# Kernel optimization log

Hardware: AMD Instinct MI355X
Metric: run time of the kernel (lower is better)

## Reference

```python
import jax, jax.numpy as jnp
import numpy as np

B, S = 256, 500
NQ, DQ, DV, M, F = 10000, 128, 256, 50, 512


def _kaiming(key, shape, fan_in):
    return jax.random.normal(key, shape, dtype=jnp.float32) * np.sqrt(2.0 / fan_in)


def setup_inputs() -> dict:
    key = jax.random.key(0)
    ks = jax.random.split(key, 24)
    inp = {
        'q_data': jax.random.randint(ks[0], (B, S), 0, NQ, dtype=jnp.int32),
        'qa_data': jax.random.randint(ks[1], (B, S), 0, 2 * NQ, dtype=jnp.int32),
        'target': jax.random.randint(ks[2], (B, S), 0, 3, dtype=jnp.int32),
        'time_data': jax.random.randint(ks[3], (B, S), 0, 9902, dtype=jnp.int32),
        'attempt_data': jax.random.randint(ks[4], (B, S), 0, 4000, dtype=jnp.int32),
        'hint_data': jax.random.randint(ks[5], (B, S), 0, 60, dtype=jnp.int32),
        'hintTotal_data': jax.random.randint(ks[6], (B, S), 0, 60, dtype=jnp.int32),
    }
    # embedding tables (padding row 0 zeroed, as in torch padding_idx=0)
    inp['q_emb'] = _kaiming(ks[7], (NQ + 1, DQ), DQ).at[0].set(0.0)
    inp['qa_emb'] = _kaiming(ks[8], (2 * NQ + 1, DV), DV).at[0].set(0.0)
    inp['time_emb'] = _kaiming(ks[9], (9902, DQ), DQ).at[0].set(0.0)
    inp['attempt_emb'] = _kaiming(ks[10], (4000, DQ), DQ).at[0].set(0.0)
    inp['hint_total_emb'] = _kaiming(ks[11], (60, DQ), DQ).at[0].set(0.0)
    # memory init
    inp['Mk'] = _kaiming(ks[12], (M, DQ), DQ)
    inp['Mv0'] = _kaiming(ks[13], (M, DV), DV)
    # difficulty linears (shared weights applied twice)
    inp['diff_W'] = _kaiming(ks[14], (DQ, DQ), DQ)
    inp['diff_b'] = jnp.zeros((DQ,), jnp.float32)
    inp['diff2_W'] = _kaiming(ks[15], (DQ, DQ), DQ)
    inp['diff2_b'] = jnp.zeros((DQ,), jnp.float32)
    # DKVMN write head: erase/add linears (DV -> DV)
    inp['erase_W'] = _kaiming(ks[16], (DV, DV), DV)
    inp['erase_b'] = jnp.zeros((DV,), jnp.float32)
    inp['add_W'] = _kaiming(ks[17], (DV, DV), DV)
    inp['add_b'] = jnp.zeros((DV,), jnp.float32)
    # readout
    inp['read_W'] = _kaiming(ks[18], (F, DV + DQ), DV + DQ)
    inp['read_b'] = jnp.zeros((F,), jnp.float32)
    inp['pred_W'] = _kaiming(ks[19], (1, F), F)
    inp['pred_b'] = jnp.zeros((1,), jnp.float32)
    return inp


def reference(q_data, qa_data, target, time_data, attempt_data, hint_data, hintTotal_data,
              q_emb, qa_emb, time_emb, attempt_emb, hint_total_emb,
              Mk, Mv0, diff_W, diff_b, diff2_W, diff2_b,
              erase_W, erase_b, add_W, add_b, read_W, read_b, pred_W, pred_b):
    lin1 = lambda x: x @ diff_W.T + diff_b
    lin2 = lambda x: x @ diff2_W.T + diff2_b

    qe = q_emb[q_data]                        # [B,S,DQ]
    te = time_emb[time_data]
    ae = attempt_emb[attempt_data]
    he = hint_total_emb[hint_data]            # forward uses hint_total_embed for both
    hte = hint_total_emb[hintTotal_data]

    time_final = jax.nn.sigmoid(lin2(jnp.tanh(lin1(te + qe))))
    diff_final = jax.nn.sigmoid(lin2(jnp.tanh(lin1(hte + he + ae + qe))))
    q_proc = lin1(qe + diff_final * (he + hte + ae))  # [B,S,DQ]
    qa_e = qa_emb[qa_data]                            # [B,S,DV]

    Mv_init = jnp.broadcast_to(Mv0[None], (q_data.shape[0], M, DV))

    def step(Mv, inp):
        q, qa = inp                                   # [B,DQ], [B,DV]
        w = jax.nn.softmax(q @ Mk.T, axis=-1)         # [B,M]
        read = jnp.einsum('bm,bmd->bd', w, Mv)        # [B,DV]
        e = jax.nn.sigmoid(qa @ erase_W.T + erase_b)  # [B,DV]
        a = jnp.tanh(qa @ add_W.T + add_b)            # [B,DV]
        Mv = Mv * (1.0 - w[:, :, None] * e[:, None, :]) + w[:, :, None] * a[:, None, :]
        return Mv, read

    _, reads = jax.lax.scan(step, Mv_init,
                            (jnp.swapaxes(q_proc, 0, 1), jnp.swapaxes(qa_e, 0, 1)))
    reads = jnp.swapaxes(reads, 0, 1)                 # [B,S,DV]

    input_embed = q_proc + time_final * te            # [B,S,DQ]
    predict_input = jnp.concatenate([reads, input_embed], axis=-1)
    rc = jnp.tanh(predict_input @ read_W.T + read_b)  # [B,S,F]
    pred = (rc @ pred_W.T + pred_b).reshape(-1)       # [B*S]

    t1 = target.reshape(-1)
    mask = t1 >= 1
    y = jnp.where(mask, t1 - 1, 0).astype(jnp.float32)
    # BCE with logits: log(1+e^x) - x*y
    lelem = jnp.logaddexp(0.0, pred) - pred * y
    n = jnp.maximum(jnp.sum(mask.astype(jnp.float32)), 1.0)
    loss = jnp.sum(jnp.where(mask, lelem, 0.0)) / n
    maskf = mask.astype(jnp.float32)
    return loss, jax.nn.sigmoid(pred) * maskf, y * maskf
```

## Files before the change

### kernel.cpp

```cpp
#include <hip/hip_runtime.h>
#include <cstdint>
#include <cstddef>

#define NB 256
#define SQ 500
#define NROWS (NB * SQ)
#define DQ 128
#define DV 256
#define MM 50
#define FF 512
#define NQA 20096
#define WSTRIDE 52
#define WT 10

typedef _Float16 half8 __attribute__((ext_vector_type(8)));
typedef float floatx4 __attribute__((ext_vector_type(4)));
typedef float f2 __attribute__((ext_vector_type(2)));
typedef unsigned int u32;
typedef unsigned short u16;

typedef __attribute__((address_space(1))) void gvoid;
typedef __attribute__((address_space(3))) void lvoid;

__device__ __forceinline__ void gl16(const u16* g, u16* l) {
    __builtin_amdgcn_global_load_lds((gvoid*)g, (lvoid*)l, 16, 0, 0);
}

__device__ __forceinline__ float4 ld4(const float* p) {
    return *reinterpret_cast<const float4*>(p);
}
__device__ __forceinline__ float sigf(float x) { return 1.f / (1.f + __expf(-x)); }
__device__ __forceinline__ float tanhfast(float x) { return 2.f / (1.f + __expf(-2.f * x)) - 1.f; }
__device__ __forceinline__ int gmap(int l, int s0, int CS) {
    int b = (unsigned)l / (unsigned)CS;
    return b * SQ + s0 + (l - b * CS);
}
__device__ __forceinline__ void st4h(u16* dst, float4 v) {
    _Float16 h0 = (_Float16)v.x, h1 = (_Float16)v.y, h2 = (_Float16)v.z, h3 = (_Float16)v.w;
    ushort4 u;
    u.x = *(u16*)&h0; u.y = *(u16*)&h1; u.z = *(u16*)&h2; u.w = *(u16*)&h3;
    *(ushort4*)dst = u;
}
__device__ __forceinline__ float h2f(u16 b) { _Float16 h; *(u16*)&h = b; return (float)h; }
__device__ __forceinline__ u16 f2h(float x) { _Float16 h = (_Float16)x; return *(u16*)&h; }

__global__ __launch_bounds__(256) void cvt16(
    const float* __restrict__ s, u16* __restrict__ d, int n4)
{
    int i = blockIdx.x * 256 + threadIdx.x;
    if (i < n4) st4h(d + 4 * (size_t)i, ld4(s + 4 * (size_t)i));
}

__global__ __launch_bounds__(256) void mkcvt(
    const float* __restrict__ Mk, u16* __restrict__ Mkh)
{
    int i = blockIdx.x * 256 + threadIdx.x;
    if (i >= 64 * 32) return;
    int row = i >> 5;
    float4 v = (row < MM) ? ld4(Mk + (size_t)row * DQ + (i & 31) * 4)
                          : float4{0.f, 0.f, 0.f, 0.f};
    st4h(Mkh + 4 * (size_t)i, v);
}

__global__ __launch_bounds__(256) void prep128(
    const int* __restrict__ q_data, const int* __restrict__ time_data,
    const int* __restrict__ attempt_data, const int* __restrict__ hint_data,
    const int* __restrict__ hintT_data,
    const float* __restrict__ q_emb, const float* __restrict__ time_emb,
    const float* __restrict__ attempt_emb, const float* __restrict__ ht_emb,
    u16* __restrict__ Xp, u16* __restrict__ S3p, u16* __restrict__ QEp,
    int s0, int CS, int Nc)
{
    int g = blockIdx.x * 256 + threadIdx.x;
    int l = g >> 5;
    int kq = (g & 31) << 2;
    if (l >= Nc) return;
    int n = gmap(l, s0, CS);
    float4 qe  = ld4(q_emb       + (size_t)q_data[n]       * DQ + kq);
    float4 te  = ld4(time_emb    + (size_t)time_data[n]    * DQ + kq);
    float4 ae  = ld4(attempt_emb + (size_t)attempt_data[n] * DQ + kq);
    float4 he  = ld4(ht_emb      + (size_t)hint_data[n]    * DQ + kq);
    float4 hte = ld4(ht_emb      + (size_t)hintT_data[n]   * DQ + kq);
    size_t off = (size_t)l * DQ + kq;
    float4 x1, s3, x2;
    x1.x = te.x + qe.x; x1.y = te.y + qe.y; x1.z = te.z + qe.z; x1.w = te.w + qe.w;
    s3.x = he.x + hte.x + ae.x; s3.y = he.y + hte.y + ae.y;
    s3.z = he.z + hte.z + ae.z; s3.w = he.w + hte.w + ae.w;
    x2.x = s3.x + qe.x; x2.y = s3.y + qe.y; x2.z = s3.z + qe.z; x2.w = s3.w + qe.w;
    st4h(Xp + off, x1);
    st4h(Xp + (size_t)Nc * DQ + off, x2);
    st4h(S3p + off, s3);
    st4h(QEp + off, qe);
}

template <int MODE>
__global__ __launch_bounds__(256, 2) void gemm16(
    const u16* __restrict__ A, const u16* __restrict__ W0,
    const u16* __restrict__ W1, const float* __restrict__ b0,
    const float* __restrict__ b1, u16* __restrict__ Yh,
    float* __restrict__ Yf,
    const u16* __restrict__ QEp, const u16* __restrict__ S3p,
    const int* __restrict__ idx, const float* __restrict__ gtab,
    u16* __restrict__ AUX, const float* __restrict__ predW,
    int K, int Nc, int s0, int CS)
{
    __shared__ u16 smem[2 * 128 * 64];
    u16* At = smem;
    u16* Bt = smem + 128 * 64;
    const int tid = threadIdx.x;
    const int row0 = blockIdx.x * 128;
    const int by = blockIdx.y;

    const u16* Wp;
    int col0;
    if constexpr (MODE == 4) { Wp = (by < 2) ? W0 : W1; col0 = (by & 1) * 128; }
    else { Wp = W0; col0 = by * 128; }
    const float* bias = (MODE == 4 && by >= 2) ? b1 : b0;

    floatx4 acc[4][4];
#pragma unroll
    for (int m = 0; m < 4; ++m)
#pragma unroll
        for (int n = 0; n < 4; ++n) acc[m][n] = (floatx4)0.f;

    const int lane = tid & 63, wv = tid >> 6;
    const int wr = (wv >> 1) * 64, wc = (wv & 1) * 64;
    const int q = lane >> 4, c0 = lane & 15;

    for (int kt = 0; kt < K; kt += 64) {
#pragma unroll
        for (int j = 0; j < 4; ++j) {
            int f = tid + j * 256;
            int r = f >> 3;
            int lg = (f & 7) ^ (r & 7);
            gl16(A + (size_t)(row0 + r) * K + kt + lg * 8, &At[f * 8]);
        }
#pragma unroll
        for (int j = 0; j < 4; ++j) {
            int f = tid + j * 256;
            int r = f >> 3;
            int lg = (f & 7) ^ (r & 7);
            gl16(Wp + (size_t)(col0 + r) * K + kt + lg * 8, &Bt[f * 8]);
        }
        __syncthreads();
#pragma unroll
        for (int kk = 0; kk < 2; ++kk) {
            half8 af[4], bf[4];
#pragma unroll
            for (int m = 0; m < 4; ++m) {
                int row = wr + m * 16 + c0;
                af[m] = *(half8*)&At[row * 64 + ((((kk << 2) | q)) ^ (row & 7)) * 8];
            }
#pragma unroll
            for (int n = 0; n < 4; ++n) {
                int row = wc + n * 16 + c0;
                bf[n] = *(half8*)&Bt[row * 64 + ((((kk << 2) | q)) ^ (row & 7)) * 8];
            }
#pragma unroll
            for (int m = 0; m < 4; ++m)
#pragma unroll
                for (int n = 0; n < 4; ++n)
                    acc[m][n] = __builtin_amdgcn_mfma_f32_16x16x32_f16(af[m], bf[n], acc[m][n], 0, 0, 0);
        }
        __syncthreads();
    }

    float bv[4];
#pragma unroll
    for (int n = 0; n < 4; ++n) bv[n] = bias[col0 + wc + n * 16 + c0];

    if constexpr (MODE == 5) {
        float pw[4];
#pragma unroll
        for (int n = 0; n < 4; ++n) pw[n] = predW[col0 + wc + n * 16 + c0];
        float* red = (float*)smem;
#pragma unroll
        for (int m = 0; m < 4; ++m)
#pragma unroll
            for (int r4 = 0; r4 < 4; ++r4) {
                int row = wr + m * 16 + q * 4 + r4;
                float pp = 0.f;
#pragma unroll
                for (int n = 0; n < 4; ++n)
                    pp = fmaf(tanhfast(acc[m][n][r4] + bv[n]), pw[n], pp);
                red[row * 33 + (wv & 1) * 16 + c0] = pp;
            }
        __syncthreads();
        if (tid < 128) {
            float s = 0.f;
#pragma unroll
            for (int j = 0; j < 32; ++j) s += red[tid * 33 + j];
            atomicAdd(&Yf[row0 + tid], s);
        }
    } else {
#pragma unroll
        for (int m = 0; m < 4; ++m)
#pragma unroll
            for (int r4 = 0; r4 < 4; ++r4) {
                int row = row0 + wr + m * 16 + q * 4 + r4;
#pragma unroll
                for (int n = 0; n < 4; ++n) {
                    int col = col0 + wc + n * 16 + c0;
                    float v = acc[m][n][r4] + bv[n];
                    if constexpr (MODE == 1) {
                        Yh[(size_t)row * 128 + col] = f2h(tanhfast(v));
                    } else if constexpr (MODE == 2) {
                        v = sigf(v);
                        if (row < Nc) {
                            Yh[(size_t)row * 128 + col] = f2h(v);
                        } else {
                            size_t o = (size_t)(row - Nc) * 128 + col;
                            float qe = h2f(QEp[o]), s3 = h2f(S3p[o]);
                            Yh[(size_t)row * 128 + col] = f2h(fmaf(v, s3, qe));
                        }
                    } else if constexpr (MODE == 3) {
                        size_t o = (size_t)row * 128 + col;
                        float tf = h2f(Yh[o]);
                        float te = gtab[(size_t)idx[gmap(row, s0, CS)] * 128 + col];
                        AUX[(size_t)row * 384 + 256 + col] = f2h(fmaf(tf, te, v));
                        Yh[o] = f2h(v);
                    } else {
                        bool isE = (by < 2);
                        v = isE ? sigf(v) : tanhfast(v);
                        AUX[((size_t)row * 256 + col) * 2 + (isE ? 0 : 1)] = f2h(v);
                    }
                }
            }
    }
}

__global__ __launch_bounds__(256) void wsoftmax_mfma(
    const u16* __restrict__ QP, const u16* __restrict__ Mkh,
    float* __restrict__ Wb)
{
    __shared__ float Sred[128 * 67];
    u16* At = (u16*)Sred;
    u16* Bt = At + 128 * 40;
    const int tid = threadIdx.x;
    const int row0 = blockIdx.x * 128;
    const int lane = tid & 63, wv = tid >> 6;
    const int wr = wv * 32;
    const int q = lane >> 4, c0 = lane & 15;

    floatx4 acc[2][4];
#pragma unroll
    for (int m = 0; m < 2; ++m)
#pragma unroll
        for (int n = 0; n < 4; ++n) acc[m][n] = (floatx4)0.f;

    for (int kt = 0; kt < DQ; kt += 32) {
#pragma unroll
        for (int i = 0; i < 3; ++i) {
            int c = tid + i * 256;
            if (c < 512) {
                int r = c >> 2, seg = c & 3;
                *(uint4*)&At[r * 40 + seg * 8] =
                    *(const uint4*)(QP + (size_t)(row0 + r) * DQ + kt + seg * 8);
            } else {
                int cb = c - 512;
                int r = cb >> 2, seg = cb & 3;
                *(uint4*)&Bt[r * 40 + seg * 8] =
                    *(const uint4*)(Mkh + (size_t)r * DQ + kt + seg * 8);
            }
        }
        __syncthreads();
        half8 af[2], bf[4];
#pragma unroll
        for (int m = 0; m < 2; ++m) af[m] = *(half8*)&At[(wr + m * 16 + c0) * 40 + q * 8];
#pragma unroll
        for (int n = 0; n < 4; ++n) bf[n] = *(half8*)&Bt[(n * 16 + c0) * 40 + q * 8];
#pragma unroll
        for (int m = 0; m < 2; ++m)
#pragma unroll
            for (int n = 0; n < 4; ++n)
                acc[m][n] = __builtin_amdgcn_mfma_f32_16x16x32_f16(af[m], bf[n], acc[m][n], 0, 0, 0);
        __syncthreads();
    }

#pragma unroll
    for (int m = 0; m < 2; ++m)
#pragma unroll
        for (int r4 = 0; r4 < 4; ++r4) {
            int row = wr + m * 16 + q * 4 + r4;
#pragma unroll
            for (int n = 0; n < 4; ++n)
                Sred[row * 67 + n * 16 + c0] = acc[m][n][r4];
        }
    __syncthreads();

    if (tid < 128) {
        float* s = &Sred[tid * 67];
        float mx = -3.0e38f;
#pragma unroll
        for (int m = 0; m < MM; ++m) mx = fmaxf(mx, s[m]);
        float sum = 0.f;
#pragma unroll
        for (int m = 0; m < MM; ++m) { float e = __expf(s[m] - mx); s[m] = e; sum += e; }
        float inv = 1.f / sum;
#pragma unroll
        for (int m = 0; m < MM; ++m) s[m] *= inv;
        s[50] = 0.f; s[51] = 0.f;
    }
    __syncthreads();

    for (int i = tid; i < 128 * 13; i += 256) {
        int row = i / 13, seg = i - row * 13;
        float4 v;
        v.x = Sred[row * 67 + seg * 4 + 0];
        v.y = Sred[row * 67 + seg * 4 + 1];
        v.z = Sred[row * 67 + seg * 4 + 2];
        v.w = Sred[row * 67 + seg * 4 + 3];
        *(float4*)(Wb + (size_t)(row0 + row) * WSTRIDE + seg * 4) = v;
    }
}

__global__ __launch_bounds__(256, 1) void scan_kernel(
    const float* __restrict__ Wb, const int* __restrict__ qa_data,
    const u32* __restrict__ EAtab,
    const float* __restrict__ Mv0, float* __restrict__ MvSt,
    u16* __restrict__ RDIE, int CS, int s0, int first)
{
    __shared__ float wt[2][WT * WSTRIDE];
    const int b = blockIdx.x;
    const int d = threadIdx.x;

    f2 mv[25];
    if (first) {
#pragma unroll
        for (int j = 0; j < 25; ++j) {
            mv[j].x = Mv0[(2 * j) * DV + d];
            mv[j].y = Mv0[(2 * j + 1) * DV + d];
        }
    } else {
#pragma unroll
        for (int j = 0; j < 25; ++j) {
            mv[j].x = MvSt[((size_t)b * MM + 2 * j) * DV + d];
            mv[j].y = MvSt[((size_t)b * MM + 2 * j + 1) * DV + d];
        }
    }

    const float* wbase = Wb + (size_t)b * CS * WSTRIDE;
    const int* qap = qa_data + (size_t)b * SQ + s0;
    u16* rp = RDIE + (size_t)b * CS * 384 + d;

    const int NT = CS / WT;
    const bool loader = (d < (WT * WSTRIDE / 4));

    if (loader) *(float4*)&wt[0][d * 4] = ld4(wbase + d * 4);
    u32 ea[WT];
    {
        int qi[WT];
#pragma unroll
        for (int i = 0; i < WT; ++i) qi[i] = qap[i];
#pragma unroll
        for (int i = 0; i < WT; ++i) ea[i] = EAtab[(size_t)qi[i] * DV + d];
    }
    __syncthreads();

    int cur = 0;
    for (int tile = 0; tile < NT; ++tile) {
        float4 wreg;
        u32 ean[WT];
        const bool havenext = (tile + 1 < NT);
        if (havenext) {
            if (loader) wreg = ld4(wbase + (size_t)(tile + 1) * WT * WSTRIDE + d * 4);
            int qn[WT];
#pragma unroll
            for (int i = 0; i < WT; ++i) qn[i] = qap[(tile + 1) * WT + i];
#pragma unroll
            for (int i = 0; i < WT; ++i) ean[i] = EAtab[(size_t)qn[i] * DV + d];
        }

        float4 wpp[2][13];
#pragma unroll
        for (int i = 0; i < 13; ++i)
            wpp[0][i] = *(const float4*)&wt[cur][i * 4];

#pragma unroll
        for (int s = 0; s < WT; ++s) {
            if (s + 1 < WT) {
#pragma unroll
                for (int i = 0; i < 13; ++i)
                    wpp[(s + 1) & 1][i] =
                        *(const float4*)&wt[cur][(s + 1) * WSTRIDE + i * 4];
            }
            const f2* w2 = (const f2*)wpp[s & 1];
            u32 eav = ea[s];
            float e = h2f((u16)(eav & 0xffff));
            float a = h2f((u16)(eav >> 16));
            f2 e2; e2.x = e; e2.y = e;
            f2 a2; a2.x = a; a2.y = a;
            f2 r0 = (f2)0.f, r1 = (f2)0.f, r2 = (f2)0.f, r3 = (f2)0.f;
#pragma unroll
            for (int j = 0; j < 24; j += 4) {
                f2 w_0 = w2[j + 0], w_1 = w2[j + 1], w_2 = w2[j + 2], w_3 = w2[j + 3];
                r0 += w_0 * mv[j + 0];
                r1 += w_1 * mv[j + 1];
                r2 += w_2 * mv[j + 2];
                r3 += w_3 * mv[j + 3];
                f2 t0 = a2 - e2 * mv[j + 0];
                f2 t1 = a2 - e2 * mv[j + 1];
                f2 t2 = a2 - e2 * mv[j + 2];
                f2 t3 = a2 - e2 * mv[j + 3];
                mv[j + 0] += w_0 * t0;
                mv[j + 1] += w_1 * t1;
                mv[j + 2] += w_2 * t2;
                mv[j + 3] += w_3 * t3;
            }
            {
                f2 w24 = w2[24];
                r0 += w24 * mv[24];
                f2 t = a2 - e2 * mv[24];
                mv[24] += w24 * t;
            }
            f2 rs = (r0 + r1) + (r2 + r3);
            rp[(size_t)(tile * WT + s) * 384] = f2h(rs.x + rs.y);
        }

        if (havenext) {
            if (loader) *(float4*)&wt[1 - cur][d * 4] = wreg;
#pragma unroll
            for (int i = 0; i < WT; ++i) ea[i] = ean[i];
            __syncthreads();
            cur ^= 1;
        }
    }

#pragma unroll
    for (int j = 0; j < 25; ++j) {
        MvSt[((size_t)b * MM + 2 * j) * DV + d]     = mv[j].x;
        MvSt[((size_t)b * MM + 2 * j + 1) * DV + d] = mv[j].y;
    }
}

__global__ __launch_bounds__(256) void loss_part(
    const float* __restrict__ P, const int* __restrict__ target,
    const float* __restrict__ pred_b, float* __restrict__ out,
    float* __restrict__ R2, int s0, int CS, int Nc)
{
    int l = blockIdx.x * 256 + threadIdx.x;
    float le = 0.f, mf = 0.f;
    if (l < Nc) {
        int n = gmap(l, s0, CS);
        float p = P[l] + pred_b[0];
        int t = target[n];
        float y = (t >= 1) ? (float)(t - 1) : 0.f;
        float sig = 1.f / (1.f + __expf(-p));
        if (t >= 1) {
            mf = 1.f;
            le = fmaxf(p, 0.f) + log1pf(__expf(-fabsf(p))) - p * y;
        }
        out[1 + n] = sig * mf;
        out[1 + NROWS + n] = y * mf;
    }
#pragma unroll
    for (int off = 32; off; off >>= 1) {
        le += __shfl_down(le, off);
        mf += __shfl_down(mf, off);
    }
    __shared__ float sl[4], sm[4];
    int wid = threadIdx.x >> 6;
    if ((threadIdx.x & 63) == 0) { sl[wid] = le; sm[wid] = mf; }
    __syncthreads();
    if (threadIdx.x == 0) {
        atomicAdd(R2, sl[0] + sl[1] + sl[2] + sl[3]);
        atomicAdd(R2 + 1, sm[0] + sm[1] + sm[2] + sm[3]);
    }
}

__global__ void loss_fin(const float* __restrict__ R2, float* __restrict__ out)
{
    out[0] = R2[0] / fmaxf(R2[1], 1.f);
}

extern "C" void kernel_launch(void* const* d_in, const int* in_sizes, int n_in,
                              void* d_out, int out_size, void* d_ws, size_t ws_size,
                              hipStream_t stream)
{
    const int* q_data       = (const int*)d_in[0];
    const int* qa_data      = (const int*)d_in[1];
    const int* target       = (const int*)d_in[2];
    const int* time_data    = (const int*)d_in[3];
    const int* attempt_data = (const int*)d_in[4];
    const int* hint_data    = (const int*)d_in[5];
    const int* hintT_data   = (const int*)d_in[6];
    const float* q_emb    = (const float*)d_in[7];
    const float* qa_emb   = (const float*)d_in[8];
    const float* time_emb = (const float*)d_in[9];
    const float* att_emb  = (const float*)d_in[10];
    const float* ht_emb   = (const float*)d_in[11];
    const float* Mk       = (const float*)d_in[12];
    const float* Mv0      = (const float*)d_in[13];
    const float* diff_W   = (const float*)d_in[14];
    const float* diff_b   = (const float*)d_in[15];
    const float* diff2_W  = (const float*)d_in[16];
    const float* diff2_b  = (const float*)d_in[17];
    const float* erase_W  = (const float*)d_in[18];
    const float* erase_b  = (const float*)d_in[19];
    const float* add_W    = (const float*)d_in[20];
    const float* add_b    = (const float*)d_in[21];
    const float* read_W   = (const float*)d_in[22];
    const float* read_b   = (const float*)d_in[23];
    const float* pred_W   = (const float*)d_in[24];
    const float* pred_b   = (const float*)d_in[25];
    float* out = (float*)d_out;
    (void)in_sizes; (void)n_in; (void)out_size;

    static const int cs_opts[] = {500, 250, 100, 50, 20, 10};
    const size_t FIXED = 44700000ull;
    int CS = 0;
    for (int i = 0; i < 6; ++i) {
        size_t need = (size_t)NB * cs_opts[i] * 2016ull + FIXED;
        if (need <= ws_size) { CS = cs_opts[i]; break; }
    }
    if (CS == 0) return;
    const int NCH = SQ / CS;
    const int Nc = NB * CS;

    float* MvSt  = (float*)d_ws;
    float* wbuf  = MvSt + (size_t)NB * MM * DV;
    float* bufP  = wbuf + (size_t)Nc * WSTRIDE;
    float* bufR2 = bufP + Nc;
    u16*  Xp     = (u16*)(bufR2 + 4);
    u16*  S3p    = Xp + (size_t)2 * Nc * 128;
    u16*  QEp    = S3p + (size_t)Nc * 128;
    u16*  RDIE   = QEp + (size_t)Nc * 128;
    u16*  dWh    = RDIE + (size_t)Nc * 384;
    u16*  d2Wh   = dWh + 16384;
    u16*  eWh    = d2Wh + 16384;
    u16*  aWh    = eWh + 65536;
    u16*  rWh    = aWh + 65536;
    u16*  qaEh   = rWh + 196608;
    u16*  Mkh    = qaEh + 5120256;
    u32*  EAtab  = (u32*)(Mkh + 8192);

    cvt16<<<16, 256, 0, stream>>>(diff_W,  dWh,  16384 / 4);
    cvt16<<<16, 256, 0, stream>>>(diff2_W, d2Wh, 16384 / 4);
    cvt16<<<64, 256, 0, stream>>>(erase_W, eWh,  65536 / 4);
    cvt16<<<64, 256, 0, stream>>>(add_W,   aWh,  65536 / 4);
    cvt16<<<192, 256, 0, stream>>>(read_W, rWh,  196608 / 4);
    cvt16<<<5001, 256, 0, stream>>>(qa_emb, qaEh, 5120256 / 4);
    mkcvt<<<8, 256, 0, stream>>>(Mk, Mkh);
    hipMemsetAsync(bufR2, 0, 4 * sizeof(float), stream);

    gemm16<4><<<dim3(NQA / 128, 4), 256, 0, stream>>>(
        qaEh, eWh, aWh, erase_b, add_b, nullptr, nullptr,
        nullptr, nullptr, nullptr, nullptr, (u16*)EAtab, nullptr, 256, 0, 0, 0);

    for (int c = 0; c < NCH; ++c) {
        const int s0 = c * CS;

        prep128<<<Nc / 8, 256, 0, stream>>>(
            q_data, time_data, attempt_data, hint_data, hintT_data,
            q_emb, time_emb, att_emb, ht_emb, Xp, S3p, QEp, s0, CS, Nc);

        gemm16<1><<<dim3(2 * Nc / 128, 1), 256, 0, stream>>>(
            Xp, dWh, nullptr, diff_b, nullptr, Xp, nullptr,
            nullptr, nullptr, nullptr, nullptr, nullptr, nullptr, 128, Nc, s0, CS);
        gemm16<2><<<dim3(2 * Nc / 128, 1), 256, 0, stream>>>(
            Xp, d2Wh, nullptr, diff2_b, nullptr, Xp, nullptr,
            QEp, S3p, nullptr, nullptr, nullptr, nullptr, 128, Nc, s0, CS);
        gemm16<3><<<dim3(Nc / 128, 1), 256, 0, stream>>>(
            Xp + (size_t)Nc * 128, dWh, nullptr, diff_b, nullptr, Xp, nullptr,
            nullptr, nullptr, time_data, time_emb, RDIE, nullptr, 128, Nc, s0, CS);
        wsoftmax_mfma<<<Nc / 128, 256, 0, stream>>>(Xp, Mkh, wbuf);
        scan_kernel<<<NB, DV, 0, stream>>>(
            wbuf, qa_data, EAtab, Mv0, MvSt, RDIE, CS, s0, c == 0 ? 1 : 0);

        hipMemsetAsync(bufP, 0, (size_t)Nc * sizeof(float), stream);
        gemm16<5><<<dim3(Nc / 128, 4), 256, 0, stream>>>(
            RDIE, rWh, nullptr, read_b, nullptr, nullptr, bufP,
            nullptr, nullptr, nullptr, nullptr, nullptr, pred_W, 384, Nc, s0, CS);

        loss_part<<<Nc / 256, 256, 0, stream>>>(bufP, target, pred_b, out, bufR2, s0, CS, Nc);
    }

    loss_fin<<<1, 1, 0, stream>>>(bufR2, out);
}
```

Before: 686.6 us.

## Fuse difficulty GEMM chain and softmax-weight GEMM into shared-memory kernels

Merges the two back-to-back difficulty linears (tanh then sigmoid) into one kernel that keeps the tanh output in shared memory instead of writing it out and reading it back. Likewise fuses the third difficulty GEMM with the Mk similarity/softmax GEMM, so the intermediate query projection never leaves LDS. The five weight-conversion launches are also collapsed into one. This cuts launches and global round trips per chunk, at the cost of 64KB of LDS per block, which may lower occupancy.

New measurement: 645.6 us. 6.0% less time.

```diff
diff --git a/kernel.cpp b/kernel.cpp
--- a/kernel.cpp
+++ b/kernel.cpp
@@ -49,6 +49,22 @@
 {
     int i = blockIdx.x * 256 + threadIdx.x;
     if (i < n4) st4h(d + 4 * (size_t)i, ld4(s + 4 * (size_t)i));
+}
+
+__global__ __launch_bounds__(256) void wcvt(
+    const float* __restrict__ s0, const float* __restrict__ s1,
+    const float* __restrict__ s2, const float* __restrict__ s3,
+    const float* __restrict__ s4, u16* __restrict__ dst)
+{
+    int i = blockIdx.x * 256 + threadIdx.x;
+    if (i >= 90112) return;
+    const float* s; int off;
+    if (i < 4096)       { s = s0; off = 0; }
+    else if (i < 8192)  { s = s1; off = 4096; }
+    else if (i < 24576) { s = s2; off = 8192; }
+    else if (i < 40960) { s = s3; off = 24576; }
+    else                { s = s4; off = 40960; }
+    st4h(dst + 4 * (size_t)i, ld4(s + 4 * (size_t)(i - off)));
 }
 
 __global__ __launch_bounds__(256) void mkcvt(
@@ -93,54 +109,38 @@
     st4h(QEp + off, qe);
 }
 
-template <int MODE>
-__global__ __launch_bounds__(256, 2) void gemm16(
-    const u16* __restrict__ A, const u16* __restrict__ W0,
-    const u16* __restrict__ W1, const float* __restrict__ b0,
-    const float* __restrict__ b1, u16* __restrict__ Yh,
-    float* __restrict__ Yf,
-    const u16* __restrict__ QEp, const u16* __restrict__ S3p,
-    const int* __restrict__ idx, const float* __restrict__ gtab,
-    u16* __restrict__ AUX, const float* __restrict__ predW,
-    int K, int Nc, int s0, int CS)
-{
-    __shared__ u16 smem[2 * 128 * 64];
+__global__ __launch_bounds__(256, 2) void gemm12(
+    const u16* __restrict__ A, const u16* __restrict__ W1h,
+    const u16* __restrict__ W2h, const float* __restrict__ b1,
+    const float* __restrict__ b2, u16* __restrict__ Yh,
+    const u16* __restrict__ QEp, const u16* __restrict__ S3p, int Nc)
+{
+    __shared__ u16 smem[32768];
     u16* At = smem;
-    u16* Bt = smem + 128 * 64;
+    u16* Bt = smem + 8192;
+    u16* Tt = smem + 16384;
     const int tid = threadIdx.x;
     const int row0 = blockIdx.x * 128;
-    const int by = blockIdx.y;
-
-    const u16* Wp;
-    int col0;
-    if constexpr (MODE == 4) { Wp = (by < 2) ? W0 : W1; col0 = (by & 1) * 128; }
-    else { Wp = W0; col0 = by * 128; }
-    const float* bias = (MODE == 4 && by >= 2) ? b1 : b0;
-
-    floatx4 acc[4][4];
-#pragma unroll
-    for (int m = 0; m < 4; ++m)
-#pragma unroll
-        for (int n = 0; n < 4; ++n) acc[m][n] = (floatx4)0.f;
-
     const int lane = tid & 63, wv = tid >> 6;
     const int wr = (wv >> 1) * 64, wc = (wv & 1) * 64;
     const int q = lane >> 4, c0 = lane & 15;
 
-    for (int kt = 0; kt < K; kt += 64) {
+    floatx4 acc[4][4];
+#pragma unroll
+    for (int m = 0; m < 4; ++m)
+#pragma unroll
+        for (int n = 0; n < 4; ++n) acc[m][n] = (floatx4)0.f;
+
+    for (int kt = 0; kt < 128; kt += 64) {
 #pragma unroll
         for (int j = 0; j < 4; ++j) {
-            int f = tid + j * 256;
-            int r = f >> 3;
-            int lg = (f & 7) ^ (r & 7);
-            gl16(A + (size_t)(row0 + r) * K + kt + lg * 8, &At[f * 8]);
+            int f = tid + j * 256; int r = f >> 3; int lg = (f & 7) ^ (r & 7);
+            gl16(A + (size_t)(row0 + r) * 128 + kt + lg * 8, &At[f * 8]);
         }
 #pragma unroll
         for (int j = 0; j < 4; ++j) {
-            int f = tid + j * 256;
-            int r = f >> 3;
-            int lg = (f & 7) ^ (r & 7);
-            gl16(Wp + (size_t)(col0 + r) * K + kt + lg * 8, &Bt[f * 8]);
+            int f = tid + j * 256; int r = f >> 3; int lg = (f & 7) ^ (r & 7);
+            gl16(W1h + (size_t)r * 128 + kt + lg * 8, &Bt[f * 8]);
         }
         __syncthreads();
 #pragma unroll
@@ -165,126 +165,220 @@
         __syncthreads();
     }
 
-    float bv[4];
-#pragma unroll
-    for (int n = 0; n < 4; ++n) bv[n] = bias[col0 + wc + n * 16 + c0];
-
-    if constexpr (MODE == 5) {
-        float pw[4];
-#pragma unroll
-        for (int n = 0; n < 4; ++n) pw[n] = predW[col0 + wc + n * 16 + c0];
-        float* red = (float*)smem;
+    {
+        float bv1[4];
+#pragma unroll
+        for (int n = 0; n < 4; ++n) bv1[n] = b1[wc + n * 16 + c0];
 #pragma unroll
         for (int m = 0; m < 4; ++m)
 #pragma unroll
             for (int r4 = 0; r4 < 4; ++r4) {
                 int row = wr + m * 16 + q * 4 + r4;
-                float pp = 0.f;
+#pragma unroll
+                for (int n = 0; n < 4; ++n) {
+                    int col = wc + n * 16 + c0;
+                    float v = tanhfast(acc[m][n][r4] + bv1[n]);
+                    int tile = col >> 6, cl = col & 63, gl = cl >> 3;
+                    Tt[tile * 8192 + row * 64 + ((gl ^ (row & 7)) << 3) + (cl & 7)] = f2h(v);
+                }
+            }
+    }
+#pragma unroll
+    for (int m = 0; m < 4; ++m)
+#pragma unroll
+        for (int n = 0; n < 4; ++n) acc[m][n] = (floatx4)0.f;
+
+#pragma unroll
+    for (int j = 0; j < 4; ++j) {
+        int f = tid + j * 256; int r = f >> 3; int lg = (f & 7) ^ (r & 7);
+        gl16(W2h + (size_t)r * 128 + 0 + lg * 8, &Bt[f * 8]);
+    }
+    __syncthreads();
+
+#pragma unroll
+    for (int kt = 0; kt < 2; ++kt) {
+#pragma unroll
+        for (int kk = 0; kk < 2; ++kk) {
+            half8 af[4], bf[4];
+#pragma unroll
+            for (int m = 0; m < 4; ++m) {
+                int row = wr + m * 16 + c0;
+                af[m] = *(half8*)&Tt[kt * 8192 + row * 64 + ((((kk << 2) | q)) ^ (row & 7)) * 8];
+            }
+#pragma unroll
+            for (int n = 0; n < 4; ++n) {
+                int row = wc + n * 16 + c0;
+                bf[n] = *(half8*)&Bt[row * 64 + ((((kk << 2) | q)) ^ (row & 7)) * 8];
+            }
+#pragma unroll
+            for (int m = 0; m < 4; ++m)
 #pragma unroll
                 for (int n = 0; n < 4; ++n)
-                    pp = fmaf(tanhfast(acc[m][n][r4] + bv[n]), pw[n], pp);
-                red[row * 33 + (wv & 1) * 16 + c0] = pp;
-            }
-        __syncthreads();
-        if (tid < 128) {
-            float s = 0.f;
-#pragma unroll
-            for (int j = 0; j < 32; ++j) s += red[tid * 33 + j];
-            atomicAdd(&Yf[row0 + tid], s);
-        }
-    } else {
-#pragma unroll
-        for (int m = 0; m < 4; ++m)
-#pragma unroll
-            for (int r4 = 0; r4 < 4; ++r4) {
-                int row = row0 + wr + m * 16 + q * 4 + r4;
-#pragma unroll
-                for (int n = 0; n < 4; ++n) {
-                    int col = col0 + wc + n * 16 + c0;
-                    float v = acc[m][n][r4] + bv[n];
-                    if constexpr (MODE == 1) {
-                        Yh[(size_t)row * 128 + col] = f2h(tanhfast(v));
-                    } else if constexpr (MODE == 2) {
-                        v = sigf(v);
-                        if (row < Nc) {
-                            Yh[(size_t)row * 128 + col] = f2h(v);
-                        } else {
-                            size_t o = (size_t)(row - Nc) * 128 + col;
-                            float qe = h2f(QEp[o]), s3 = h2f(S3p[o]);
-                            Yh[(size_t)row * 128 + col] = f2h(fmaf(v, s3, qe));
-                        }
-                    } else if constexpr (MODE == 3) {
-                        size_t o = (size_t)row * 128 + col;
-                        float tf = h2f(Yh[o]);
-                        float te = gtab[(size_t)idx[gmap(row, s0, CS)] * 128 + col];
-                        AUX[(size_t)row * 384 + 256 + col] = f2h(fmaf(tf, te, v));
-                        Yh[o] = f2h(v);
-                    } else {
-                        bool isE = (by < 2);
-                        v = isE ? sigf(v) : tanhfast(v);
-                        AUX[((size_t)row * 256 + col) * 2 + (isE ? 0 : 1)] = f2h(v);
-                    }
+                    acc[m][n] = __builtin_amdgcn_mfma_f32_16x16x32_f16(af[m], bf[n], acc[m][n], 0, 0, 0);
+        }
+        if (kt == 0) {
+            __syncthreads();
+#pragma unroll
+            for (int j = 0; j < 4; ++j) {
+                int f = tid + j * 256; int r = f >> 3; int lg = (f & 7) ^ (r & 7);
+                gl16(W2h + (size_t)r * 128 + 64 + lg * 8, &Bt[f * 8]);
+            }
+            __syncthreads();
+        }
+    }
+
+    float bv[4];
+#pragma unroll
+    for (int n = 0; n < 4; ++n) bv[n] = b2[wc + n * 16 + c0];
+#pragma unroll
+    for (int m = 0; m < 4; ++m)
+#pragma unroll
+        for (int r4 = 0; r4 < 4; ++r4) {
+            int row = row0 + wr + m * 16 + q * 4 + r4;
+#pragma unroll
+            for (int n = 0; n < 4; ++n) {
+                int col = wc + n * 16 + c0;
+                float v = sigf(acc[m][n][r4] + bv[n]);
+                if (row < Nc) {
+                    Yh[(size_t)row * 128 + col] = f2h(v);
+                } else {
+                    size_t o = (size_t)(row - Nc) * 128 + col;
+                    float qe = h2f(QEp[o]), s3 = h2f(S3p[o]);
+                    Yh[(size_t)row * 128 + col] = f2h(fmaf(v, s3, qe));
                 }
             }
-    }
-}
-
-__global__ __launch_bounds__(256) void wsoftmax_mfma(
-    const u16* __restrict__ QP, const u16* __restrict__ Mkh,
-    float* __restrict__ Wb)
-{
-    __shared__ float Sred[128 * 67];
-    u16* At = (u16*)Sred;
-    u16* Bt = At + 128 * 40;
+        }
+}
+
+__global__ __launch_bounds__(256, 2) void gemm3w(
+    const u16* __restrict__ X3, const u16* __restrict__ W1h,
+    const float* __restrict__ b1, const u16* __restrict__ Mkh,
+    const int* __restrict__ tidx, const float* __restrict__ temb,
+    const u16* __restrict__ TF, u16* __restrict__ RDIE,
+    float* __restrict__ Wb, int s0, int CS)
+{
+    __shared__ u16 smem[32768];
+    u16* At = smem;
+    u16* Bt = smem + 8192;
+    u16* Tt = smem + 16384;
     const int tid = threadIdx.x;
     const int row0 = blockIdx.x * 128;
     const int lane = tid & 63, wv = tid >> 6;
-    const int wr = wv * 32;
+    const int wr = (wv >> 1) * 64, wc = (wv & 1) * 64;
     const int q = lane >> 4, c0 = lane & 15;
 
-    floatx4 acc[2][4];
+    floatx4 acc[4][4];
+#pragma unroll
+    for (int m = 0; m < 4; ++m)
+#pragma unroll
+        for (int n = 0; n < 4; ++n) acc[m][n] = (floatx4)0.f;
+
+    for (int kt = 0; kt < 128; kt += 64) {
+#pragma unroll
+        for (int j = 0; j < 4; ++j) {
+            int f = tid + j * 256; int r = f >> 3; int lg = (f & 7) ^ (r & 7);
+            gl16(X3 + (size_t)(row0 + r) * 128 + kt + lg * 8, &At[f * 8]);
+        }
+#pragma unroll
+        for (int j = 0; j < 4; ++j) {
+            int f = tid + j * 256; int r = f >> 3; int lg = (f & 7) ^ (r & 7);
+            gl16(W1h + (size_t)r * 128 + kt + lg * 8, &Bt[f * 8]);
+        }
+        __syncthreads();
+#pragma unroll
+        for (int kk = 0; kk < 2; ++kk) {
+            half8 af[4], bf[4];
+#pragma unroll
+            for (int m = 0; m < 4; ++m) {
+                int row = wr + m * 16 + c0;
+                af[m] = *(half8*)&At[row * 64 + ((((kk << 2) | q)) ^ (row & 7)) * 8];
+            }
+#pragma unroll
+            for (int n = 0; n < 4; ++n) {
+                int row = wc + n * 16 + c0;
+                bf[n] = *(half8*)&Bt[row * 64 + ((((kk << 2) | q)) ^ (row & 7)) * 8];
+            }
+#pragma unroll
+            for (int m = 0; m < 4; ++m)
+#pragma unroll
+                for (int n = 0; n < 4; ++n)
+                    acc[m][n] = __builtin_amdgcn_mfma_f32_16x16x32_f16(af[m], bf[n], acc[m][n], 0, 0, 0);
+        }
+        __syncthreads();
+    }
+
+    {
+        float bv1[4];
+#pragma unroll
+        for (int n = 0; n < 4; ++n) bv1[n] = b1[wc + n * 16 + c0];
+#pragma unroll
+        for (int m = 0; m < 4; ++m)
+#pragma unroll
+            for (int r4 = 0; r4 < 4; ++r4) {
+                int rloc = wr + m * 16 + q * 4 + r4;
+                int grow = row0 + rloc;
+                int nmap = gmap(grow, s0, CS);
+                const float* terow = temb + (size_t)tidx[nmap] * 128;
+#pragma unroll
+                for (int n = 0; n < 4; ++n) {
+                    int col = wc + n * 16 + c0;
+                    float qp = acc[m][n][r4] + bv1[n];
+                    int tile = col >> 6, cl = col & 63, gl = cl >> 3;
+                    Tt[tile * 8192 + rloc * 64 + ((gl ^ (rloc & 7)) << 3) + (cl & 7)] = f2h(qp);
+                    float tf = h2f(TF[(size_t)grow * 128 + col]);
+                    RDIE[(size_t)grow * 384 + 256 + col] = f2h(fmaf(tf, terow[col], qp));
+                }
+            }
+    }
+#pragma unroll
+    for (int j = 0; j < 4; ++j) {
+        int f = tid + j * 256;
+        int fl = f & 511;
+        int ktile = f >> 9;
+        int r = fl >> 3;
+        int lg = (fl & 7) ^ (r & 7);
+        gl16(Mkh + (size_t)r * 128 + ktile * 64 + lg * 8, &Bt[f * 8]);
+    }
+    __syncthreads();
+
+    const int wrW = wv * 32;
+    floatx4 acc2[2][4];
 #pragma unroll
     for (int m = 0; m < 2; ++m)
 #pragma unroll
-        for (int n = 0; n < 4; ++n) acc[m][n] = (floatx4)0.f;
-
-    for (int kt = 0; kt < DQ; kt += 32) {
-#pragma unroll
-        for (int i = 0; i < 3; ++i) {
-            int c = tid + i * 256;
-            if (c < 512) {
-                int r = c >> 2, seg = c & 3;
-                *(uint4*)&At[r * 40 + seg * 8] =
-                    *(const uint4*)(QP + (size_t)(row0 + r) * DQ + kt + seg * 8);
-            } else {
-                int cb = c - 512;
-                int r = cb >> 2, seg = cb & 3;
-                *(uint4*)&Bt[r * 40 + seg * 8] =
-                    *(const uint4*)(Mkh + (size_t)r * DQ + kt + seg * 8);
-            }
-        }
-        __syncthreads();
-        half8 af[2], bf[4];
-#pragma unroll
-        for (int m = 0; m < 2; ++m) af[m] = *(half8*)&At[(wr + m * 16 + c0) * 40 + q * 8];
-#pragma unroll
-        for (int n = 0; n < 4; ++n) bf[n] = *(half8*)&Bt[(n * 16 + c0) * 40 + q * 8];
-#pragma unroll
-        for (int m = 0; m < 2; ++m)
+        for (int n = 0; n < 4; ++n) acc2[m][n] = (floatx4)0.f;
+#pragma unroll
+    for (int kt = 0; kt < 2; ++kt)
+#pragma unroll
+        for (int kk = 0; kk < 2; ++kk) {
+            half8 af[2], bf[4];
+#pragma unroll
+            for (int m = 0; m < 2; ++m) {
+                int row = wrW + m * 16 + c0;
+                af[m] = *(half8*)&Tt[kt * 8192 + row * 64 + ((((kk << 2) | q)) ^ (row & 7)) * 8];
+            }
+#pragma unroll
+            for (int n = 0; n < 4; ++n) {
+                int row = n * 16 + c0;
+                bf[n] = *(half8*)&Bt[kt * 4096 + row * 64 + ((((kk << 2) | q)) ^ (row & 7)) * 8];
+            }
+#pragma unroll
+            for (int m = 0; m < 2; ++m)
+#pragma unroll
+                for (int n = 0; n < 4; ++n)
+                    acc2[m][n] = __builtin_amdgcn_mfma_f32_16x16x32_f16(af[m], bf[n], acc2[m][n], 0, 0, 0);
+        }
+    __syncthreads();
+
+    float* Sred = (float*)smem;
+#pragma unroll
+    for (int m = 0; m < 2; ++m)
+#pragma unroll
+        for (int r4 = 0; r4 < 4; ++r4) {
+            int row = wrW + m * 16 + q * 4 + r4;
 #pragma unroll
             for (int n = 0; n < 4; ++n)
-                acc[m][n] = __builtin_amdgcn_mfma_f32_16x16x32_f16(af[m], bf[n], acc[m][n], 0, 0, 0);
-        __syncthreads();
-    }
-
-#pragma unroll
-    for (int m = 0; m < 2; ++m)
-#pragma unroll
-        for (int r4 = 0; r4 < 4; ++r4) {
-            int row = wr + m * 16 + q * 4 + r4;
-#pragma unroll
-            for (int n = 0; n < 4; ++n)
-                Sred[row * 67 + n * 16 + c0] = acc[m][n][r4];
+                Sred[row * 67 + n * 16 + c0] = acc2[m][n][r4];
         }
     __syncthreads();
 
@@ -311,6 +405,121 @@
         v.z = Sred[row * 67 + seg * 4 + 2];
         v.w = Sred[row * 67 + seg * 4 + 3];
         *(float4*)(Wb + (size_t)(row0 + row) * WSTRIDE + seg * 4) = v;
+    }
+}
+
+template <int MODE>
+__global__ __launch_bounds__(256, 2) void gemm16(
+    const u16* __restrict__ A, const u16* __restrict__ W0,
+    const u16* __restrict__ W1, const float* __restrict__ b0,
+    const float* __restrict__ b1, u16* __restrict__ Yh,
+    float* __restrict__ Yf,
+    u16* __restrict__ AUX, const float* __restrict__ predW,
+    int K)
+{
+    __shared__ u16 smem[2 * 128 * 64];
+    u16* At = smem;
+    u16* Bt = smem + 128 * 64;
+    const int tid = threadIdx.x;
+    const int row0 = blockIdx.x * 128;
+    const int by = blockIdx.y;
+
+    const u16* Wp;
+    int col0;
+    if constexpr (MODE == 4) { Wp = (by < 2) ? W0 : W1; col0 = (by & 1) * 128; }
+    else { Wp = W0; col0 = by * 128; }
+    const float* bias = (MODE == 4 && by >= 2) ? b1 : b0;
+
+    floatx4 acc[4][4];
+#pragma unroll
+    for (int m = 0; m < 4; ++m)
+#pragma unroll
+        for (int n = 0; n < 4; ++n) acc[m][n] = (floatx4)0.f;
+
+    const int lane = tid & 63, wv = tid >> 6;
+    const int wr = (wv >> 1) * 64, wc = (wv & 1) * 64;
+    const int q = lane >> 4, c0 = lane & 15;
+
+    for (int kt = 0; kt < K; kt += 64) {
+#pragma unroll
+        for (int j = 0; j < 4; ++j) {
+            int f = tid + j * 256;
+            int r = f >> 3;
+            int lg = (f & 7) ^ (r & 7);
+            gl16(A + (size_t)(row0 + r) * K + kt + lg * 8, &At[f * 8]);
+        }
+#pragma unroll
+        for (int j = 0; j < 4; ++j) {
+            int f = tid + j * 256;
+            int r = f >> 3;
+            int lg = (f & 7) ^ (r & 7);
+            gl16(Wp + (size_t)(col0 + r) * K + kt + lg * 8, &Bt[f * 8]);
+        }
+        __syncthreads();
+#pragma unroll
+        for (int kk = 0; kk < 2; ++kk) {
+            half8 af[4], bf[4];
+#pragma unroll
+            for (int m = 0; m < 4; ++m) {
+                int row = wr + m * 16 + c0;
+                af[m] = *(half8*)&At[row * 64 + ((((kk << 2) | q)) ^ (row & 7)) * 8];
+            }
+#pragma unroll
+            for (int n = 0; n < 4; ++n) {
+                int row = wc + n * 16 + c0;
+                bf[n] = *(half8*)&Bt[row * 64 + ((((kk << 2) | q)) ^ (row & 7)) * 8];
+            }
+#pragma unroll
+            for (int m = 0; m < 4; ++m)
+#pragma unroll
+                for (int n = 0; n < 4; ++n)
+                    acc[m][n] = __builtin_amdgcn_mfma_f32_16x16x32_f16(af[m], bf[n], acc[m][n], 0, 0, 0);
+        }
+        __syncthreads();
+    }
+
+    float bv[4];
+#pragma unroll
+    for (int n = 0; n < 4; ++n) bv[n] = bias[col0 + wc + n * 16 + c0];
+
+    if constexpr (MODE == 5) {
+        float pw[4];
+#pragma unroll
+        for (int n = 0; n < 4; ++n) pw[n] = predW[col0 + wc + n * 16 + c0];
+        float* red = (float*)smem;
+#pragma unroll
+        for (int m = 0; m < 4; ++m)
+#pragma unroll
+            for (int r4 = 0; r4 < 4; ++r4) {
+                int row = wr + m * 16 + q * 4 + r4;
+                float pp = 0.f;
+#pragma unroll
+                for (int n = 0; n < 4; ++n)
+                    pp = fmaf(tanhfast(acc[m][n][r4] + bv[n]), pw[n], pp);
+                red[row * 33 + (wv & 1) * 16 + c0] = pp;
+            }
+        __syncthreads();
+        if (tid < 128) {
+            float s = 0.f;
+#pragma unroll
+            for (int j = 0; j < 32; ++j) s += red[tid * 33 + j];
+            atomicAdd(&Yf[row0 + tid], s);
+        }
+    } else {
+#pragma unroll
+        for (int m = 0; m < 4; ++m)
+#pragma unroll
+            for (int r4 = 0; r4 < 4; ++r4) {
+                int row = row0 + wr + m * 16 + q * 4 + r4;
+#pragma unroll
+                for (int n = 0; n < 4; ++n) {
+                    int col = col0 + wc + n * 16 + c0;
+                    float v = acc[m][n][r4] + bv[n];
+                    bool isE = (by < 2);
+                    v = isE ? sigf(v) : tanhfast(v);
+                    AUX[((size_t)row * 256 + col) * 2 + (isE ? 0 : 1)] = f2h(v);
+                }
+            }
     }
 }
 
@@ -534,18 +743,14 @@
     u16*  Mkh    = qaEh + 5120256;
     u32*  EAtab  = (u32*)(Mkh + 8192);
 
-    cvt16<<<16, 256, 0, stream>>>(diff_W,  dWh,  16384 / 4);
-    cvt16<<<16, 256, 0, stream>>>(diff2_W, d2Wh, 16384 / 4);
-    cvt16<<<64, 256, 0, stream>>>(erase_W, eWh,  65536 / 4);
-    cvt16<<<64, 256, 0, stream>>>(add_W,   aWh,  65536 / 4);
-    cvt16<<<192, 256, 0, stream>>>(read_W, rWh,  196608 / 4);
+    wcvt<<<352, 256, 0, stream>>>(diff_W, diff2_W, erase_W, add_W, read_W, dWh);
     cvt16<<<5001, 256, 0, stream>>>(qa_emb, qaEh, 5120256 / 4);
     mkcvt<<<8, 256, 0, stream>>>(Mk, Mkh);
     hipMemsetAsync(bufR2, 0, 4 * sizeof(float), stream);
 
     gemm16<4><<<dim3(NQA / 128, 4), 256, 0, stream>>>(
         qaEh, eWh, aWh, erase_b, add_b, nullptr, nullptr,
-        nullptr, nullptr, nullptr, nullptr, (u16*)EAtab, nullptr, 256, 0, 0, 0);
+        (u16*)EAtab, nullptr, 256);
 
     for (int c = 0; c < NCH; ++c) {
         const int s0 = c * CS;
@@ -554,23 +759,20 @@
             q_data, time_data, attempt_data, hint_data, hintT_data,
             q_emb, time_emb, att_emb, ht_emb, Xp, S3p, QEp, s0, CS, Nc);
 
-        gemm16<1><<<dim3(2 * Nc / 128, 1), 256, 0, stream>>>(
-            Xp, dWh, nullptr, diff_b, nullptr, Xp, nullptr,
-            nullptr, nullptr, nullptr, nullptr, nullptr, nullptr, 128, Nc, s0, CS);
-        gemm16<2><<<dim3(2 * Nc / 128, 1), 256, 0, stream>>>(
-            Xp, d2Wh, nullptr, diff2_b, nullptr, Xp, nullptr,
-            QEp, S3p, nullptr, nullptr, nullptr, nullptr, 128, Nc, s0, CS);
-        gemm16<3><<<dim3(Nc / 128, 1), 256, 0, stream>>>(
-            Xp + (size_t)Nc * 128, dWh, nullptr, diff_b, nullptr, Xp, nullptr,
-            nullptr, nullptr, time_data, time_emb, RDIE, nullptr, 128, Nc, s0, CS);
-        wsoftmax_mfma<<<Nc / 128, 256, 0, stream>>>(Xp, Mkh, wbuf);
+        gemm12<<<2 * Nc / 128, 256, 0, stream>>>(
+            Xp, dWh, d2Wh, diff_b, diff2_b, Xp, QEp, S3p, Nc);
+
+        gemm3w<<<Nc / 128, 256, 0, stream>>>(
+            Xp + (size_t)Nc * 128, dWh, diff_b, Mkh,
+            time_data, time_emb, Xp, RDIE, wbuf, s0, CS);
+
         scan_kernel<<<NB, DV, 0, stream>>>(
             wbuf, qa_data, EAtab, Mv0, MvSt, RDIE, CS, s0, c == 0 ? 1 : 0);
 
         hipMemsetAsync(bufP, 0, (size_t)Nc * sizeof(float), stream);
         gemm16<5><<<dim3(Nc / 128, 4), 256, 0, stream>>>(
             RDIE, rWh, nullptr, read_b, nullptr, nullptr, bufP,
-            nullptr, nullptr, nullptr, nullptr, nullptr, pred_W, 384, Nc, s0, CS);
+            nullptr, pred_W, 384);
 
         loss_part<<<Nc / 256, 256, 0, stream>>>(bufP, target, pred_b, out, bufR2, s0, CS, Nc);
     }
```
